# Kernel tuning notes

Measured on AMD Instinct MI355X. Metric: run time of the kernel, lower is better.

The kernel has to match this reference:

```python
import math
import jax, jax.numpy as jnp
import numpy as np
from jax.scipy.special import xlogy, gammaln


def get_positional_embed(seq_len, feature_size):
    # Enformer-style relative positional basis over distances [-(L-1), L-1].
    distances = jnp.arange(-seq_len + 1, seq_len, dtype=jnp.float32)  # [2L-1]
    n = feature_size // 6
    absd = jnp.abs(distances)[:, None]  # [2L-1, 1]

    # exponential basis
    max_range = math.log(seq_len) / math.log(2.0)
    half_life = 2.0 ** jnp.linspace(3.0, max_range, n)  # [n]
    feat_exp = jnp.exp(-math.log(2.0) / half_life[None, :] * absd)

    # central mask basis
    center_widths = 2.0 ** jnp.arange(1, n + 1, dtype=jnp.float32) - 1.0
    feat_cm = (center_widths[None, :] > absd).astype(jnp.float32)

    # gamma pdf basis
    stddev = seq_len / (2.0 * n)
    start_mean = seq_len / n
    mean = jnp.linspace(start_mean, float(seq_len), n)[None, :]
    conc = (mean / stddev) ** 2
    rate = mean / stddev ** 2
    log_unnorm = xlogy(conc - 1.0, absd) - rate * absd
    log_norm = gammaln(conc) - conc * jnp.log(rate)
    probs = jnp.exp(log_unnorm - log_norm) + 1e-8
    feat_gamma = probs / jnp.max(probs, axis=-1, keepdims=True)

    emb = jnp.concatenate([feat_exp, feat_cm, feat_gamma], axis=-1)  # [2L-1, 3n]
    emb = jnp.concatenate([emb, jnp.sign(distances)[:, None] * emb], axis=-1)  # [2L-1, 6n]
    return emb


def relative_shift(x):
    # x: [B, H, Q, 2K-1] -> [B, H, Q, K]
    b, h, t1, t2m1 = x.shape
    x = jnp.pad(x, ((0, 0), (0, 0), (0, 0), (1, 0)))  # [B,H,Q,2K]
    t2 = t2m1 + 1
    x = x.reshape(b, h, t2, t1)
    x = x[:, :, 1:, :]
    x = x.reshape(b, h, t1, t2 - 1)
    return x[..., : (t2 + 1) // 2]


def setup_inputs() -> dict:
    key = jax.random.key(0)
    ks = jax.random.split(key, 9)
    B, L, D = 2, 1024, 1024
    H, Dk, Dv = 8, 128, 128
    R = 192  # n_rel_pos_features
    sq = math.sqrt(2.0 / (D + Dk))
    sv = math.sqrt(2.0 / (D + Dv))
    return {
        "q": jax.random.normal(ks[0], (B, L, D), jnp.float32),
        "w_qs": jax.random.normal(ks[1], (D, H * Dk), jnp.float32) * sq,
        "w_ks": jax.random.normal(ks[2], (D, H * Dk), jnp.float32) * sq,
        "w_vs": jax.random.normal(ks[3], (D, H * Dv), jnp.float32) * sv,
        "w_rel_pos_k": jax.random.normal(ks[4], (R, H * Dk), jnp.float32) * 0.05,
        "rel_embed_bias": jax.random.normal(ks[5], (1, H, 1, Dk), jnp.float32),
        "rel_pos_bias": jax.random.normal(ks[6], (1, H, 1, Dk), jnp.float32),
        "w_out": jax.random.normal(ks[7], (H * Dv, D), jnp.float32) * 0.02,
        "b_out": jax.random.normal(ks[8], (D,), jnp.float32) * 0.02,
    }


def reference(q, w_qs, w_ks, w_vs, w_rel_pos_k, rel_embed_bias, rel_pos_bias, w_out, b_out):
    B, L, _ = q.shape
    H, Dk = rel_embed_bias.shape[1], rel_embed_bias.shape[3]
    Dv = w_vs.shape[1] // H
    scale = Dk ** (-0.5)

    Q = (q @ w_qs).reshape(B, L, H, Dk).transpose(0, 2, 1, 3) * scale  # [B,H,L,Dk]
    K = (q @ w_ks).reshape(B, L, H, Dk).transpose(0, 2, 1, 3)
    V = (q @ w_vs).reshape(B, L, H, Dv).transpose(0, 2, 1, 3)

    attn = jnp.einsum('bnqd,bnkd->bnqk', Q + rel_embed_bias, K)

    positions = get_positional_embed(L, w_rel_pos_k.shape[0])  # [2L-1, R]
    rel_k = (positions @ w_rel_pos_k).reshape(-1, H, Dk).transpose(1, 0, 2)  # [H,2L-1,Dk]
    attn_pos = jnp.einsum('bnqd,nkd->bnqk', Q + rel_pos_bias, rel_k)  # [B,H,L,2L-1]
    attn_pos = relative_shift(attn_pos)  # [B,H,L,L]

    a = jax.nn.softmax(attn + attn_pos, axis=-1)
    out = jnp.einsum('bnqk,bnkd->bnqd', a, V)
    out = out.transpose(0, 2, 1, 3).reshape(B, L, H * Dv)
    return out @ w_out + b_out
```

## Files before the change

kernel.cpp:

```cpp
#include <hip/hip_runtime.h>
#include <hip/hip_fp16.h>

typedef __attribute__((ext_vector_type(8))) _Float16 f16x8;
typedef __attribute__((ext_vector_type(4))) float f32x4;

#define MFMA16(a, b, c) __builtin_amdgcn_mfma_f32_16x16x32_f16((a), (b), (c), 0, 0, 0)

__device__ __forceinline__ unsigned short f2h(float f) {
  __half h = __float2half(f);
  return __half_as_ushort(h);
}

__device__ __forceinline__ void gll16(const void* g, void* l) {
  __builtin_amdgcn_global_load_lds(
      (const __attribute__((address_space(1))) unsigned int*)g,
      (__attribute__((address_space(3))) unsigned int*)l, 16, 0, 0);
}

__global__ void cvt_f16_kernel(const float* __restrict__ X, unsigned short* __restrict__ Y) {
  size_t i = ((size_t)blockIdx.x * blockDim.x + threadIdx.x) * 4;
  float4 v = *reinterpret_cast<const float4*>(X + i);
  ushort4 o;
  o.x = f2h(v.x); o.y = f2h(v.y); o.z = f2h(v.z); o.w = f2h(v.w);
  *reinterpret_cast<ushort4*>(Y + i) = o;
}

__global__ void transpose_w4_kernel(const float* __restrict__ W0, const float* __restrict__ W1,
                                    const float* __restrict__ W2, const float* __restrict__ W3,
                                    unsigned short* __restrict__ T0, unsigned short* __restrict__ T1,
                                    unsigned short* __restrict__ T2, unsigned short* __restrict__ T3) {
  __shared__ float tile[32][33];
  int z = blockIdx.z;
  const float* W = (z == 0) ? W0 : ((z == 1) ? W1 : ((z == 2) ? W2 : W3));
  unsigned short* WT = (z == 0) ? T0 : ((z == 1) ? T1 : ((z == 2) ? T2 : T3));
  int c0 = blockIdx.x * 32, r0 = blockIdx.y * 32;
  int tx = threadIdx.x, ty = threadIdx.y;
#pragma unroll
  for (int i = 0; i < 32; i += 8)
    tile[ty + i][tx] = W[(size_t)(r0 + ty + i) * 1024 + c0 + tx];
  __syncthreads();
#pragma unroll
  for (int i = 0; i < 32; i += 8)
    WT[(size_t)(c0 + ty + i) * 1024 + r0 + tx] = f2h(tile[tx][ty + i]);
}

__global__ void transpose_wr_kernel(const float* __restrict__ W, unsigned short* __restrict__ WT) {
  __shared__ float tile[32][33];
  int c0 = blockIdx.x * 32, r0 = blockIdx.y * 32;
  int tx = threadIdx.x, ty = threadIdx.y;
#pragma unroll
  for (int i = 0; i < 32; i += 8)
    tile[ty + i][tx] = W[(size_t)(r0 + ty + i) * 1024 + c0 + tx];
  __syncthreads();
#pragma unroll
  for (int i = 0; i < 32; i += 8)
    WT[(size_t)(c0 + ty + i) * 192 + r0 + tx] = f2h(tile[tx][ty + i]);
}

__global__ void posembed_kernel(unsigned short* __restrict__ pos) {
  int grp = (blockIdx.x * blockDim.x + threadIdx.x) >> 5;
  int j = threadIdx.x & 31;
  if (grp >= 2048) return;
  unsigned short* row = pos + (size_t)grp * 192;
  if (grp == 2047) {
#pragma unroll
    for (int t = 0; t < 6; ++t) row[t * 32 + j] = 0;
    return;
  }
  float dist = (float)grp - 1023.0f;
  float absd = fabsf(dist);
  float jp = (float)(j + 1);
  float hl = exp2f(3.0f + (float)j * (7.0f / 31.0f));
  float fe = exp2f(-absd / hl);
  float cw = exp2f(jp) - 1.0f;
  float fc = (cw > absd) ? 1.0f : 0.0f;
  float conc = 4.0f * jp * jp;
  float rate = 0.125f * jp;
  float lu = (conc - 1.0f) * logf(absd) - rate * absd;
  float ln_ = lgammaf(conc) - conc * logf(rate);
  float p = expf(lu - ln_) + 1e-8f;
  float mp = p;
#pragma unroll
  for (int off = 16; off >= 1; off >>= 1) mp = fmaxf(mp, __shfl_xor(mp, off));
  float gm = p / mp;
  unsigned short e = f2h(fe), c = f2h(fc), gg = f2h(gm);
  row[j] = e; row[32 + j] = c; row[64 + j] = gg;
  unsigned short se, sc, sg;
  if (dist > 0.0f)      { se = e; sc = c; sg = gg; }
  else if (dist < 0.0f) { se = (unsigned short)(e ^ 0x8000u);
                          sc = (unsigned short)(c ^ 0x8000u);
                          sg = (unsigned short)(gg ^ 0x8000u); }
  else                  { se = 0; sc = 0; sg = 0; }
  row[96 + j] = se; row[128 + j] = sc; row[160 + j] = sg;
}

__global__ __launch_bounds__(256) void gemm16_kernel(
    const unsigned short* __restrict__ A, const unsigned short* __restrict__ A3,
    const unsigned short* __restrict__ BT0, const unsigned short* __restrict__ BT1,
    const unsigned short* __restrict__ BT2, const unsigned short* __restrict__ BT3,
    unsigned short* __restrict__ D0, unsigned short* __restrict__ D1,
    unsigned short* __restrict__ D2, unsigned short* __restrict__ D3,
    int Kmain, int K3) {
  __shared__ unsigned short As[128][64];
  __shared__ unsigned short Bs[128][64];
  int z = blockIdx.z;
  const unsigned short* Az = (z == 3) ? A3 : A;
  const unsigned short* BT = (z == 0) ? BT0 : ((z == 1) ? BT1 : ((z == 2) ? BT2 : BT3));
  unsigned short* D = (z == 0) ? D0 : ((z == 1) ? D1 : ((z == 2) ? D2 : D3));
  int K = (z == 3) ? K3 : Kmain;
  const int N = 1024;

  int tid = threadIdx.x, wave = tid >> 6, lane = tid & 63;
  int g = lane >> 4, r16 = lane & 15;
  int wr = wave >> 1, wc = wave & 1;
  int m0 = blockIdx.x * 128, n0 = blockIdx.y * 128;
  int srow = wave * 32 + (lane >> 3);
  int scb = lane & 7;

  f32x4 acc[4][4] = {};

  for (int k0 = 0; k0 < K; k0 += 64) {
    __syncthreads();
#pragma unroll
    for (int i = 0; i < 4; ++i) {
      int row = srow + i * 8;
      int cb = scb ^ (row & 7);
      gll16(Az + (size_t)(m0 + row) * K + k0 + cb * 8, &As[row][scb * 8]);
      gll16(BT + (size_t)(n0 + row) * K + k0 + cb * 8, &Bs[row][scb * 8]);
    }
    asm volatile("s_waitcnt vmcnt(0)" ::: "memory");
    __syncthreads();

    f16x8 af[2][4], bfr[2][4];
#pragma unroll
    for (int kf = 0; kf < 2; ++kf) {
#pragma unroll
      for (int mt = 0; mt < 4; ++mt) {
        int R = wr * 64 + mt * 16 + r16;
        af[kf][mt] = *reinterpret_cast<const f16x8*>(&As[R][(((kf * 4 + g)) ^ (R & 7)) * 8]);
      }
#pragma unroll
      for (int nt = 0; nt < 4; ++nt) {
        int R = wc * 64 + nt * 16 + r16;
        bfr[kf][nt] = *reinterpret_cast<const f16x8*>(&Bs[R][(((kf * 4 + g)) ^ (R & 7)) * 8]);
      }
    }
#pragma unroll
    for (int kf = 0; kf < 2; ++kf)
#pragma unroll
      for (int mt = 0; mt < 4; ++mt)
#pragma unroll
        for (int nt = 0; nt < 4; ++nt)
          acc[mt][nt] = MFMA16(af[kf][mt], bfr[kf][nt], acc[mt][nt]);
  }

#pragma unroll
  for (int nt = 0; nt < 4; ++nt) {
    int col = n0 + wc * 64 + nt * 16 + r16;
#pragma unroll
    for (int mt = 0; mt < 4; ++mt) {
      int rowb = m0 + wr * 64 + mt * 16 + g * 4;
#pragma unroll
      for (int rg = 0; rg < 4; ++rg)
        D[(size_t)(rowb + rg) * N + col] = f2h(acc[mt][nt][rg]);
    }
  }
}

__global__ void bias_init_kernel(const float* __restrict__ b, float* __restrict__ out) {
  size_t i = ((size_t)blockIdx.x * 256 + threadIdx.x) * 4;
  float4 bv = *reinterpret_cast<const float4*>(b + (i & 1023));
  *reinterpret_cast<float4*>(out + i) = bv;
}

__global__ __launch_bounds__(256) void gemm16_atomic_kernel(
    const unsigned short* __restrict__ A, const unsigned short* __restrict__ BT,
    float* __restrict__ C) {
  __shared__ unsigned short As[128][64];
  __shared__ unsigned short Bs[128][64];
  const int N = 1024, K = 1024;
  int tid = threadIdx.x, wave = tid >> 6, lane = tid & 63;
  int g = lane >> 4, r16 = lane & 15;
  int wr = wave >> 1, wc = wave & 1;
  int m0 = blockIdx.x * 128, n0 = blockIdx.y * 128;
  int kb = blockIdx.z * 512;
  int srow = wave * 32 + (lane >> 3);
  int scb = lane & 7;

  f32x4 acc[4][4] = {};

  for (int k0 = kb; k0 < kb + 512; k0 += 64) {
    __syncthreads();
#pragma unroll
    for (int i = 0; i < 4; ++i) {
      int row = srow + i * 8;
      int cb = scb ^ (row & 7);
      gll16(A + (size_t)(m0 + row) * K + k0 + cb * 8, &As[row][scb * 8]);
      gll16(BT + (size_t)(n0 + row) * K + k0 + cb * 8, &Bs[row][scb * 8]);
    }
    asm volatile("s_waitcnt vmcnt(0)" ::: "memory");
    __syncthreads();

    f16x8 af[2][4], bfr[2][4];
#pragma unroll
    for (int kf = 0; kf < 2; ++kf) {
#pragma unroll
      for (int mt = 0; mt < 4; ++mt) {
        int R = wr * 64 + mt * 16 + r16;
        af[kf][mt] = *reinterpret_cast<const f16x8*>(&As[R][(((kf * 4 + g)) ^ (R & 7)) * 8]);
      }
#pragma unroll
      for (int nt = 0; nt < 4; ++nt) {
        int R = wc * 64 + nt * 16 + r16;
        bfr[kf][nt] = *reinterpret_cast<const f16x8*>(&Bs[R][(((kf * 4 + g)) ^ (R & 7)) * 8]);
      }
    }
#pragma unroll
    for (int kf = 0; kf < 2; ++kf)
#pragma unroll
      for (int mt = 0; mt < 4; ++mt)
#pragma unroll
        for (int nt = 0; nt < 4; ++nt)
          acc[mt][nt] = MFMA16(af[kf][mt], bfr[kf][nt], acc[mt][nt]);
  }

#pragma unroll
  for (int nt = 0; nt < 4; ++nt) {
    int col = n0 + wc * 64 + nt * 16 + r16;
#pragma unroll
    for (int mt = 0; mt < 4; ++mt) {
      int rowb = m0 + wr * 64 + mt * 16 + g * 4;
#pragma unroll
      for (int rg = 0; rg < 4; ++rg)
        atomicAdd(&C[(size_t)(rowb + rg) * N + col], acc[mt][nt][rg]);
    }
  }
}

__global__ void vt_prep_kernel(const unsigned short* __restrict__ Vh, unsigned short* __restrict__ Vt) {
  __shared__ unsigned short tile[32][34];
  int bh = blockIdx.z;
  int b = bh >> 3, h = bh & 7;
  int l0 = blockIdx.x * 32, n0 = blockIdx.y * 32;
  int tx = threadIdx.x, ty = threadIdx.y;
#pragma unroll
  for (int i = 0; i < 32; i += 8)
    tile[ty + i][tx] = Vh[(size_t)(b * 1024 + l0 + ty + i) * 1024 + h * 128 + n0 + tx];
  __syncthreads();
#pragma unroll
  for (int i = 0; i < 32; i += 8)
    Vt[(size_t)bh * 131072 + (size_t)(n0 + ty + i) * 1024 + l0 + tx] = tile[tx][ty + i];
}

__global__ __launch_bounds__(256) void attn_kernel(
    const unsigned short* __restrict__ Qh, const unsigned short* __restrict__ Kh,
    const unsigned short* __restrict__ Vt, const unsigned short* __restrict__ relkh,
    const float* __restrict__ eb, const float* __restrict__ pb,
    unsigned short* __restrict__ Opart, float* __restrict__ mlpart) {
  __shared__ unsigned short Ks[2][32 * 128];
  __shared__ unsigned short Rs[128 * 128];
  __shared__ unsigned short Vs[2][128][40];
  __shared__ unsigned short Ps[4][16][40];

  int tid = threadIdx.x;
  int wave = tid >> 6, lane = tid & 63;
  int g = lane >> 4, r16 = lane & 15;

  int lin = blockIdx.x + 16 * (blockIdx.y + 2 * blockIdx.z);
  int swz = (lin & 7) * 64 + (lin >> 3);
  int ks = (swz >> 4) & 1;
  int bh = swz >> 5;
  int b = bh >> 3, h = bh & 7;
  int q0 = (swz & 15) * 64;
  int q0w = q0 + wave * 16;
  const float scale = 0.0883883476483184f;

  f16x8 qa[4], qbv[4];
  {
    int qrow = b * 1024 + q0w + r16;
    const unsigned short* qp = Qh + (size_t)qrow * 1024 + h * 128;
    const float* ebp = eb + h * 128;
    const float* pbp = pb + h * 128;
#pragma unroll
    for (int kf = 0; kf < 4; ++kf) {
      int dbase = kf * 32 + g * 8;
      uint4 qv = *reinterpret_cast<const uint4*>(qp + dbase);
      const __half* hv = reinterpret_cast<const __half*>(&qv);
      float4 e0 = *reinterpret_cast<const float4*>(ebp + dbase);
      float4 e1 = *reinterpret_cast<const float4*>(ebp + dbase + 4);
      float4 c0 = *reinterpret_cast<const float4*>(pbp + dbase);
      float4 c1 = *reinterpret_cast<const float4*>(pbp + dbase + 4);
      float ev[8] = {e0.x, e0.y, e0.z, e0.w, e1.x, e1.y, e1.z, e1.w};
      float bv[8] = {c0.x, c0.y, c0.z, c0.w, c1.x, c1.y, c1.z, c1.w};
      unsigned short ta[8], tb[8];
#pragma unroll
      for (int i = 0; i < 8; ++i) {
        float s = __half2float(hv[i]) * scale;
        ta[i] = f2h(s + ev[i]);
        tb[i] = f2h(s + bv[i]);
      }
      qa[kf] = *reinterpret_cast<f16x8*>(ta);
      qbv[kf] = *reinterpret_cast<f16x8*>(tb);
    }
  }

  float m_run[4], l_part[4];
#pragma unroll
  for (int rg = 0; rg < 4; ++rg) { m_run[rg] = -1e30f; l_part[rg] = 0.0f; }
  f32x4 o_acc[8] = {};

  const unsigned short* KB = Kh + ((size_t)b * 1024) * 1024 + h * 128;
  const unsigned short* VB = Vt + (size_t)bh * 131072;
  const unsigned short* RB = relkh + h * 128;
  int wb = 48 - wave * 16;

  const int t0 = ks * 16, t1 = t0 + 16;
  const int rb0 = 960 + t0 * 32 - q0;

  uint4 va, vb2;
#pragma unroll
  for (int i = 0; i < 2; ++i) {
    int j = i * 256 + tid;
    int row = j >> 4, s = j & 15, c = s ^ (row & 7);
    gll16(KB + (size_t)(t0 * 32 + row) * 1024 + c * 8, &Ks[t0 & 1][(row * 16 + s) * 8]);
  }
#pragma unroll
  for (int i = 0; i < 6; ++i) {
    int j = i * 256 + tid;
    int row = rb0 + (j >> 4);
    int s = j & 15, c = s ^ (row & 7);
    gll16(RB + (size_t)row * 1024 + c * 8, &Rs[(((row & 127) * 16) + s) * 8]);
  }
  {
    const unsigned short* src = VB + (size_t)(tid >> 1) * 1024 + t0 * 32 + (tid & 1) * 16;
    va = *reinterpret_cast<const uint4*>(src);
    vb2 = *reinterpret_cast<const uint4*>(src + 8);
  }

  for (int t = t0; t < t1; ++t) {
    int cur = t & 1;
    asm volatile("s_waitcnt vmcnt(0)" ::: "memory");
    {
      int rr = tid >> 1, cc = (tid & 1) * 16;
      *reinterpret_cast<uint4*>(&Vs[cur][rr][cc]) = va;
      *reinterpret_cast<uint4*>(&Vs[cur][rr][cc + 8]) = vb2;
    }
    __syncthreads();

    if (t + 1 < t1) {
      int nk0 = (t + 1) * 32;
#pragma unroll
      for (int i = 0; i < 2; ++i) {
        int j = i * 256 + tid;
        int row = j >> 4, s = j & 15, c = s ^ (row & 7);
        gll16(KB + (size_t)(nk0 + row) * 1024 + c * 8, &Ks[(t + 1) & 1][(row * 16 + s) * 8]);
      }
      int rnew = rb0 + 96 + (t - t0) * 32;
#pragma unroll
      for (int i = 0; i < 2; ++i) {
        int j = i * 256 + tid;
        int row = rnew + (j >> 4);
        int s = j & 15, c = s ^ (row & 7);
        gll16(RB + (size_t)row * 1024 + c * 8, &Rs[(((row & 127) * 16) + s) * 8]);
      }
      const unsigned short* src = VB + (size_t)(tid >> 1) * 1024 + nk0 + (tid & 1) * 16;
      va = *reinterpret_cast<const uint4*>(src);
      vb2 = *reinterpret_cast<const uint4*>(src + 8);
    }

    int rbt = rb0 + (t - t0) * 32;
    f32x4 s0 = {0.f, 0.f, 0.f, 0.f}, s1 = {0.f, 0.f, 0.f, 0.f};
    f32x4 w0 = {0.f, 0.f, 0.f, 0.f}, w1 = {0.f, 0.f, 0.f, 0.f}, w2 = {0.f, 0.f, 0.f, 0.f};
#pragma unroll
    for (int kf = 0; kf < 4; ++kf) {
      int sl = kf * 4 + g;
      int x = sl ^ (r16 & 7);
      f16x8 kb0 = *reinterpret_cast<const f16x8*>(&Ks[cur][(r16 * 16 + x) * 8]);
      f16x8 kb1 = *reinterpret_cast<const f16x8*>(&Ks[cur][((16 + r16) * 16 + x) * 8]);
      s0 = MFMA16(qa[kf], kb0, s0);
      s1 = MFMA16(qa[kf], kb1, s1);
      int R0 = rbt + wb + r16, R1 = R0 + 16, R2 = R0 + 32;
      f16x8 rb_0 = *reinterpret_cast<const f16x8*>(&Rs[((R0 & 127) * 16 + (sl ^ (R0 & 7))) * 8]);
      f16x8 rb_1 = *reinterpret_cast<const f16x8*>(&Rs[((R1 & 127) * 16 + (sl ^ (R1 & 7))) * 8]);
      f16x8 rb_2 = *reinterpret_cast<const f16x8*>(&Rs[((R2 & 127) * 16 + (sl ^ (R2 & 7))) * 8]);
      w0 = MFMA16(qbv[kf], rb_0, w0);
      w1 = MFMA16(qbv[kf], rb_1, w1);
      w2 = MFMA16(qbv[kf], rb_2, w2);
    }

    float sv[2][4];
#pragma unroll
    for (int rg = 0; rg < 4; ++rg) {
      int qp = g * 4 + rg;
      int idx = r16 + 15 - qp;
      int srcl = (lane & 48) | (idx & 15);
      float a0 = __shfl(w0[rg], srcl);
      float a1 = __shfl(w1[rg], srcl);
      float a2 = __shfl(w2[rg], srcl);
      bool lo = idx < 16;
      sv[0][rg] = s0[rg] + (lo ? a0 : a1);
      sv[1][rg] = s1[rg] + (lo ? a1 : a2);
    }

    float d = -1e30f;
#pragma unroll
    for (int rg = 0; rg < 4; ++rg)
      d = fmaxf(d, fmaxf(sv[0][rg], sv[1][rg]) - m_run[rg]);
    if (!__all(d <= 8.0f)) {
#pragma unroll
      for (int rg = 0; rg < 4; ++rg) {
        float mx = fmaxf(sv[0][rg], sv[1][rg]);
#pragma unroll
        for (int off = 8; off >= 1; off >>= 1) mx = fmaxf(mx, __shfl_xor(mx, off));
        float mnew = fmaxf(m_run[rg], mx);
        float scl = __expf(m_run[rg] - mnew);
        l_part[rg] *= scl;
#pragma unroll
        for (int nf = 0; nf < 8; ++nf) o_acc[nf][rg] *= scl;
        m_run[rg] = mnew;
      }
    }
#pragma unroll
    for (int rg = 0; rg < 4; ++rg) {
      float e0 = __expf(sv[0][rg] - m_run[rg]);
      float e1 = __expf(sv[1][rg] - m_run[rg]);
      l_part[rg] += e0 + e1;
      Ps[wave][g * 4 + rg][r16] = f2h(e0);
      Ps[wave][g * 4 + rg][16 + r16] = f2h(e1);
    }
    f16x8 pf = *reinterpret_cast<const f16x8*>(&Ps[wave][r16][g * 8]);
#pragma unroll
    for (int nf = 0; nf < 8; ++nf) {
      f16x8 vb = *reinterpret_cast<const f16x8*>(&Vs[cur][nf * 16 + r16][g * 8]);
      o_acc[nf] = MFMA16(pf, vb, o_acc[nf]);
    }
  }

  float l_run[4];
#pragma unroll
  for (int rg = 0; rg < 4; ++rg) {
    float rs = l_part[rg];
#pragma unroll
    for (int off = 8; off >= 1; off >>= 1) rs += __shfl_xor(rs, off);
    l_run[rg] = rs;
  }

  size_t slice = (size_t)(ks * 16 + bh);
#pragma unroll
  for (int rg = 0; rg < 4; ++rg) {
    unsigned short* op = Opart + (slice * 1024 + q0w + g * 4 + rg) * 128;
#pragma unroll
    for (int nf = 0; nf < 8; ++nf) op[nf * 16 + r16] = f2h(o_acc[nf][rg]);
  }
  if (r16 == 0) {
#pragma unroll
    for (int rg = 0; rg < 4; ++rg) {
      float2 ml = {m_run[rg], l_run[rg]};
      *reinterpret_cast<float2*>(mlpart + (slice * 1024 + q0w + g * 4 + rg) * 2) = ml;
    }
  }
}

__global__ void combine_kernel(const unsigned short* __restrict__ Opart,
                               const float* __restrict__ mlpart,
                               unsigned short* __restrict__ attnO) {
  int idx = blockIdx.x * 256 + threadIdx.x;
  int d4 = (idx & 31) * 4;
  int qq = (idx >> 5) & 1023;
  int bh = idx >> 15;
  float2 ml[2];
  float m = -1e30f;
#pragma unroll
  for (int s = 0; s < 2; ++s) {
    ml[s] = *reinterpret_cast<const float2*>(mlpart + (((size_t)(s * 16 + bh)) * 1024 + qq) * 2);
    m = fmaxf(m, ml[s].x);
  }
  float num0 = 0.f, num1 = 0.f, num2 = 0.f, num3 = 0.f, den = 0.f;
#pragma unroll
  for (int s = 0; s < 2; ++s) {
    float w = __expf(ml[s].x - m);
    den += w * ml[s].y;
    ushort4 ov = *reinterpret_cast<const ushort4*>(
        Opart + (((size_t)(s * 16 + bh)) * 1024 + qq) * 128 + d4);
    num0 += w * __half2float(__ushort_as_half(ov.x));
    num1 += w * __half2float(__ushort_as_half(ov.y));
    num2 += w * __half2float(__ushort_as_half(ov.z));
    num3 += w * __half2float(__ushort_as_half(ov.w));
  }
  float inv = 1.0f / den;
  ushort4 o;
  o.x = f2h(num0 * inv); o.y = f2h(num1 * inv);
  o.z = f2h(num2 * inv); o.w = f2h(num3 * inv);
  int b = bh >> 3, h = bh & 7;
  *reinterpret_cast<ushort4*>(attnO + ((size_t)(b * 1024 + qq)) * 1024 + h * 128 + d4) = o;
}

extern "C" void kernel_launch(void* const* d_in, const int* in_sizes, int n_in,
                              void* d_out, int out_size, void* d_ws, size_t ws_size,
                              hipStream_t stream) {
  const float* q      = (const float*)d_in[0];
  const float* w_qs   = (const float*)d_in[1];
  const float* w_ks   = (const float*)d_in[2];
  const float* w_vs   = (const float*)d_in[3];
  const float* w_rel  = (const float*)d_in[4];
  const float* ebias  = (const float*)d_in[5];
  const float* pbias  = (const float*)d_in[6];
  const float* w_out  = (const float*)d_in[7];
  const float* b_out  = (const float*)d_in[8];
  float* out = (float*)d_out;

  char* ws = (char*)d_ws;
  const size_t MB = 1u << 20;
  unsigned short* Xh    = (unsigned short*)(ws + 0 * MB);
  unsigned short* WqsT  = (unsigned short*)(ws + 4 * MB);
  unsigned short* WksT  = (unsigned short*)(ws + 6 * MB);
  unsigned short* WvsT  = (unsigned short*)(ws + 8 * MB);
  unsigned short* WoutT = (unsigned short*)(ws + 10 * MB);
  unsigned short* WrelT = (unsigned short*)(ws + 12 * MB);
  unsigned short* pos   = (unsigned short*)(ws + 13 * MB);
  unsigned short* Qh    = (unsigned short*)(ws + 14 * MB);
  unsigned short* Kh    = (unsigned short*)(ws + 18 * MB);
  unsigned short* Vh    = (unsigned short*)(ws + 22 * MB);
  unsigned short* relkh = (unsigned short*)(ws + 26 * MB);
  unsigned short* Vt    = (unsigned short*)(ws + 30 * MB);
  unsigned short* attnO = (unsigned short*)(ws + 34 * MB);
  unsigned short* Opart = (unsigned short*)(ws + 38 * MB);
  float* mlpart         = (float*)(ws + 50 * MB);

  cvt_f16_kernel<<<2048, 256, 0, stream>>>(q, Xh);
  transpose_w4_kernel<<<dim3(32, 32, 4), dim3(32, 8), 0, stream>>>(
      w_qs, w_ks, w_vs, w_out, WqsT, WksT, WvsT, WoutT);
  transpose_wr_kernel<<<dim3(32, 6), dim3(32, 8), 0, stream>>>(w_rel, WrelT);
  posembed_kernel<<<256, 256, 0, stream>>>(pos);

  gemm16_kernel<<<dim3(16, 8, 4), 256, 0, stream>>>(
      Xh, pos, WqsT, WksT, WvsT, WrelT, Qh, Kh, Vh, relkh, 1024, 192);

  vt_prep_kernel<<<dim3(32, 4, 16), dim3(32, 8), 0, stream>>>(Vh, Vt);

  attn_kernel<<<dim3(16, 2, 16), 256, 0, stream>>>(Qh, Kh, Vt, relkh, ebias, pbias,
                                                   Opart, mlpart);
  combine_kernel<<<2048, 256, 0, stream>>>(Opart, mlpart, attnO);

  bias_init_kernel<<<2048, 256, 0, stream>>>(b_out, out);
  gemm16_atomic_kernel<<<dim3(16, 8, 2), 256, 0, stream>>>(attnO, WoutT, out);
}
```

Baseline: 111.5 us.

## Software-pipeline score MFMAs of the next tile with softmax of the current

Restructures the attention inner loop into a two-stage software pipeline with ping-pong score accumulators (SA/SB). The QK and relative-position MFMAs for tile t+1 are issued before the shuffle, softmax and PV work of tile t, so matrix-core work can overlap with the VALU, exp and shuffle phase. The loop is manually unrolled by two, with a prologue and epilogue that keep the K, R and V double buffers consistent. The extra live accumulators raise VGPR pressure, which could lower occupancy or cause spills.

```diff
diff --git a/kernel.cpp b/kernel.cpp
--- a/kernel.cpp
+++ b/kernel.cpp
@@ -318,90 +318,71 @@
   const int rb0 = 960 + t0 * 32 - q0;
 
   uint4 va, vb2;
-#pragma unroll
-  for (int i = 0; i < 2; ++i) {
-    int j = i * 256 + tid;
-    int row = j >> 4, s = j & 15, c = s ^ (row & 7);
-    gll16(KB + (size_t)(t0 * 32 + row) * 1024 + c * 8, &Ks[t0 & 1][(row * 16 + s) * 8]);
-  }
-#pragma unroll
-  for (int i = 0; i < 6; ++i) {
-    int j = i * 256 + tid;
-    int row = rb0 + (j >> 4);
-    int s = j & 15, c = s ^ (row & 7);
-    gll16(RB + (size_t)row * 1024 + c * 8, &Rs[(((row & 127) * 16) + s) * 8]);
-  }
-  {
-    const unsigned short* src = VB + (size_t)(tid >> 1) * 1024 + t0 * 32 + (tid & 1) * 16;
+
+  auto issue_tile = [&](int t) {
+    int nk0 = t * 32;
+#pragma unroll
+    for (int i = 0; i < 2; ++i) {
+      int j = i * 256 + tid;
+      int row = j >> 4, s = j & 15, c = s ^ (row & 7);
+      gll16(KB + (size_t)(nk0 + row) * 1024 + c * 8, &Ks[t & 1][(row * 16 + s) * 8]);
+    }
+    int rnew = rb0 + 96 + (t - 1 - t0) * 32;
+#pragma unroll
+    for (int i = 0; i < 2; ++i) {
+      int j = i * 256 + tid;
+      int row = rnew + (j >> 4);
+      int s = j & 15, c = s ^ (row & 7);
+      gll16(RB + (size_t)row * 1024 + c * 8, &Rs[(((row & 127) * 16) + s) * 8]);
+    }
+    const unsigned short* src = VB + (size_t)(tid >> 1) * 1024 + nk0 + (tid & 1) * 16;
     va = *reinterpret_cast<const uint4*>(src);
     vb2 = *reinterpret_cast<const uint4*>(src + 8);
-  }
-
-  for (int t = t0; t < t1; ++t) {
+  };
+
+  auto write_v = [&](int buf) {
+    int rr = tid >> 1, cc = (tid & 1) * 16;
+    *reinterpret_cast<uint4*>(&Vs[buf][rr][cc]) = va;
+    *reinterpret_cast<uint4*>(&Vs[buf][rr][cc + 8]) = vb2;
+  };
+
+  auto mfma_phase = [&](int t, f32x4* S) {
     int cur = t & 1;
-    asm volatile("s_waitcnt vmcnt(0)" ::: "memory");
-    {
-      int rr = tid >> 1, cc = (tid & 1) * 16;
-      *reinterpret_cast<uint4*>(&Vs[cur][rr][cc]) = va;
-      *reinterpret_cast<uint4*>(&Vs[cur][rr][cc + 8]) = vb2;
-    }
-    __syncthreads();
-
-    if (t + 1 < t1) {
-      int nk0 = (t + 1) * 32;
-#pragma unroll
-      for (int i = 0; i < 2; ++i) {
-        int j = i * 256 + tid;
-        int row = j >> 4, s = j & 15, c = s ^ (row & 7);
-        gll16(KB + (size_t)(nk0 + row) * 1024 + c * 8, &Ks[(t + 1) & 1][(row * 16 + s) * 8]);
-      }
-      int rnew = rb0 + 96 + (t - t0) * 32;
-#pragma unroll
-      for (int i = 0; i < 2; ++i) {
-        int j = i * 256 + tid;
-        int row = rnew + (j >> 4);
-        int s = j & 15, c = s ^ (row & 7);
-        gll16(RB + (size_t)row * 1024 + c * 8, &Rs[(((row & 127) * 16) + s) * 8]);
-      }
-      const unsigned short* src = VB + (size_t)(tid >> 1) * 1024 + nk0 + (tid & 1) * 16;
-      va = *reinterpret_cast<const uint4*>(src);
-      vb2 = *reinterpret_cast<const uint4*>(src + 8);
-    }
-
     int rbt = rb0 + (t - t0) * 32;
-    f32x4 s0 = {0.f, 0.f, 0.f, 0.f}, s1 = {0.f, 0.f, 0.f, 0.f};
-    f32x4 w0 = {0.f, 0.f, 0.f, 0.f}, w1 = {0.f, 0.f, 0.f, 0.f}, w2 = {0.f, 0.f, 0.f, 0.f};
+#pragma unroll
+    for (int x5 = 0; x5 < 5; ++x5) S[x5] = f32x4{0.f, 0.f, 0.f, 0.f};
 #pragma unroll
     for (int kf = 0; kf < 4; ++kf) {
       int sl = kf * 4 + g;
       int x = sl ^ (r16 & 7);
       f16x8 kb0 = *reinterpret_cast<const f16x8*>(&Ks[cur][(r16 * 16 + x) * 8]);
       f16x8 kb1 = *reinterpret_cast<const f16x8*>(&Ks[cur][((16 + r16) * 16 + x) * 8]);
-      s0 = MFMA16(qa[kf], kb0, s0);
-      s1 = MFMA16(qa[kf], kb1, s1);
+      S[0] = MFMA16(qa[kf], kb0, S[0]);
+      S[1] = MFMA16(qa[kf], kb1, S[1]);
       int R0 = rbt + wb + r16, R1 = R0 + 16, R2 = R0 + 32;
       f16x8 rb_0 = *reinterpret_cast<const f16x8*>(&Rs[((R0 & 127) * 16 + (sl ^ (R0 & 7))) * 8]);
       f16x8 rb_1 = *reinterpret_cast<const f16x8*>(&Rs[((R1 & 127) * 16 + (sl ^ (R1 & 7))) * 8]);
       f16x8 rb_2 = *reinterpret_cast<const f16x8*>(&Rs[((R2 & 127) * 16 + (sl ^ (R2 & 7))) * 8]);
-      w0 = MFMA16(qbv[kf], rb_0, w0);
-      w1 = MFMA16(qbv[kf], rb_1, w1);
-      w2 = MFMA16(qbv[kf], rb_2, w2);
-    }
-
+      S[2] = MFMA16(qbv[kf], rb_0, S[2]);
+      S[3] = MFMA16(qbv[kf], rb_1, S[3]);
+      S[4] = MFMA16(qbv[kf], rb_2, S[4]);
+    }
+  };
+
+  auto process_tile = [&](f32x4* S, const unsigned short(*Vb)[40]) {
     float sv[2][4];
 #pragma unroll
     for (int rg = 0; rg < 4; ++rg) {
       int qp = g * 4 + rg;
       int idx = r16 + 15 - qp;
       int srcl = (lane & 48) | (idx & 15);
-      float a0 = __shfl(w0[rg], srcl);
-      float a1 = __shfl(w1[rg], srcl);
-      float a2 = __shfl(w2[rg], srcl);
+      float a0 = __shfl(S[2][rg], srcl);
+      float a1 = __shfl(S[3][rg], srcl);
+      float a2 = __shfl(S[4][rg], srcl);
       bool lo = idx < 16;
-      sv[0][rg] = s0[rg] + (lo ? a0 : a1);
-      sv[1][rg] = s1[rg] + (lo ? a1 : a2);
-    }
-
+      sv[0][rg] = S[0][rg] + (lo ? a0 : a1);
+      sv[1][rg] = S[1][rg] + (lo ? a1 : a2);
+    }
     float d = -1e30f;
 #pragma unroll
     for (int rg = 0; rg < 4; ++rg)
@@ -431,10 +412,65 @@
     f16x8 pf = *reinterpret_cast<const f16x8*>(&Ps[wave][r16][g * 8]);
 #pragma unroll
     for (int nf = 0; nf < 8; ++nf) {
-      f16x8 vb = *reinterpret_cast<const f16x8*>(&Vs[cur][nf * 16 + r16][g * 8]);
-      o_acc[nf] = MFMA16(pf, vb, o_acc[nf]);
-    }
-  }
+      f16x8 vv = *reinterpret_cast<const f16x8*>(&Vb[nf * 16 + r16][g * 8]);
+      o_acc[nf] = MFMA16(pf, vv, o_acc[nf]);
+    }
+  };
+
+  f32x4 SA[5], SB[5];
+
+#pragma unroll
+  for (int i = 0; i < 2; ++i) {
+    int j = i * 256 + tid;
+    int row = j >> 4, s = j & 15, c = s ^ (row & 7);
+    gll16(KB + (size_t)(t0 * 32 + row) * 1024 + c * 8, &Ks[t0 & 1][(row * 16 + s) * 8]);
+  }
+#pragma unroll
+  for (int i = 0; i < 6; ++i) {
+    int j = i * 256 + tid;
+    int row = rb0 + (j >> 4);
+    int s = j & 15, c = s ^ (row & 7);
+    gll16(RB + (size_t)row * 1024 + c * 8, &Rs[(((row & 127) * 16) + s) * 8]);
+  }
+  {
+    const unsigned short* src = VB + (size_t)(tid >> 1) * 1024 + t0 * 32 + (tid & 1) * 16;
+    va = *reinterpret_cast<const uint4*>(src);
+    vb2 = *reinterpret_cast<const uint4*>(src + 8);
+  }
+
+  asm volatile("s_waitcnt vmcnt(0)" ::: "memory");
+  __syncthreads();
+  write_v(0);
+  issue_tile(t0 + 1);
+  mfma_phase(t0, SA);
+
+  for (int i = 0; i < 7; ++i) {
+    int tb = t0 + 1 + 2 * i;
+    asm volatile("s_waitcnt vmcnt(0)" ::: "memory");
+    __syncthreads();
+    write_v(1);
+    issue_tile(tb + 1);
+    mfma_phase(tb, SB);
+    process_tile(SA, Vs[0]);
+
+    int ta = tb + 1;
+    asm volatile("s_waitcnt vmcnt(0)" ::: "memory");
+    __syncthreads();
+    write_v(0);
+    issue_tile(ta + 1);
+    mfma_phase(ta, SA);
+    process_tile(SB, Vs[1]);
+  }
+
+  {
+    int tb = t0 + 15;
+    asm volatile("s_waitcnt vmcnt(0)" ::: "memory");
+    __syncthreads();
+    write_v(1);
+    mfma_phase(tb, SB);
+    process_tile(SA, Vs[0]);
+  }
+  process_tile(SB, Vs[1]);
 
   float l_run[4];
 #pragma unroll
```

Result: slower. 126.1 us (+13.1%).
